# Performance work log

Measured on AMD Instinct MI355X. Metric: run time of the kernel, lower is better.

Reference implementation:

```python
import jax, jax.numpy as jnp
import numpy as np

B, S, D, NH, NKV, HD = 1, 2048, 4096, 32, 8, 128
SCALE = HD ** -0.5


def setup_inputs() -> dict:
    key = jax.random.key(0)
    ks = jax.random.split(key, 5)
    sd = D ** -0.5
    x = jax.random.normal(ks[0], (B, S, D), jnp.float32)
    Wq = jax.random.normal(ks[1], (D, NH * HD), jnp.float32) * sd
    Wk = jax.random.normal(ks[2], (D, NKV * HD), jnp.float32) * sd
    Wv = jax.random.normal(ks[3], (D, NKV * HD), jnp.float32) * sd
    Wo = jax.random.normal(ks[4], (NH * HD, D), jnp.float32) * sd
    # real rotary tables (rotate-half convention), shape [S, HD]
    inv_freq = 1.0 / (10000.0 ** (np.arange(0, HD, 2, dtype=np.float64) / HD))
    ang = np.outer(np.arange(S, dtype=np.float64), inv_freq)  # [S, HD//2]
    emb = np.concatenate([ang, ang], axis=-1)  # [S, HD]
    cos = jnp.asarray(np.cos(emb), jnp.float32)
    sin = jnp.asarray(np.sin(emb), jnp.float32)
    return dict(x=x, Wq=Wq, Wk=Wk, Wv=Wv, Wo=Wo, cos=cos, sin=sin)


def _rope(t, cos, sin):
    # t: [B,S,H,HD]; cos/sin: [S,HD]
    c = cos[None, :, None, :]
    s = sin[None, :, None, :]
    t1, t2 = jnp.split(t, 2, axis=-1)
    rot = jnp.concatenate([-t2, t1], axis=-1)
    return t * c + rot * s


def _to_i8(t):
    # per-vector absmax quantization over last dim
    scale = 127.0 / jnp.clip(jnp.max(jnp.abs(t), axis=-1, keepdims=True), 1e-5, None)
    q = jnp.clip(jnp.round(t * scale), -128.0, 127.0).astype(jnp.int8)
    return q, scale


def reference(x, Wq, Wk, Wv, Wo, cos, sin):
    q = (x @ Wq).reshape(B, S, NH, HD)
    k = (x @ Wk).reshape(B, S, NKV, HD)
    v = (x @ Wv).reshape(B, S, NKV, HD)
    q = _rope(q, cos, sin)
    k = _rope(k, cos, sin)
    q_i8, q_s = _to_i8(q)          # [B,S,NH,HD], [B,S,NH,1]
    k_i8, k_s = _to_i8(k)          # [B,S,NKV,HD], [B,S,NKV,1]
    rep = NH // NKV                # GQA expansion
    k_i8 = jnp.repeat(k_i8, rep, axis=2)
    k_s = jnp.repeat(k_s, rep, axis=2)
    v = jnp.repeat(v, rep, axis=2)
    # int8 QK^T accumulated in int32 (exact), then per-vector dequant
    scores = jnp.einsum('bshd,bthd->bhst', q_i8, k_i8,
                        preferred_element_type=jnp.int32).astype(jnp.float32)
    q_st = jnp.transpose(q_s, (0, 2, 1, 3))            # [B,NH,S,1]
    k_st = jnp.transpose(k_s, (0, 2, 3, 1))            # [B,NH,1,S]
    scores = scores * (SCALE / (q_st * k_st))
    # causal mask (seq > 1, no cache so total == S)
    mask = jnp.triu(jnp.full((S, S), -jnp.inf, jnp.float32), k=1)
    scores = scores + mask
    attn = jax.nn.softmax(scores, axis=-1)             # [B,NH,S,S]
    out = jnp.einsum('bhst,bthd->bshd', attn, v).reshape(B, S, NH * HD)
    return out @ Wo
```

## Files before the change

kernel.cpp:

```cpp
#include <hip/hip_runtime.h>
#include <hip/hip_bf16.h>

#define S_LEN 2048
#define DMODEL 4096
#define NH 32
#define NKV 8
#define HD 128
#define NQKV 6144
#define VOFF (DMODEL + NKV * HD)
#define ATT_SCALE_L2E 0.1275175213528852f

typedef __bf16 bf16x8 __attribute__((ext_vector_type(8)));
typedef __bf16 bf16x4 __attribute__((ext_vector_type(4)));
typedef float f32x4 __attribute__((ext_vector_type(4)));

template <bool B> struct BoolC { static constexpr bool value = B; };

__device__ __forceinline__ unsigned short f2b(float f) {
  union { float f; unsigned u; } a; a.f = f;
  unsigned u = a.u;
  return (unsigned short)((u + 0x7FFFu + ((u >> 16) & 1u)) >> 16);
}
__device__ __forceinline__ float b2f(unsigned short u) {
  union { unsigned u; float f; } a; a.u = (unsigned)u << 16; return a.f;
}

__device__ __forceinline__ void gl16(const unsigned short* g, unsigned short* l) {
  __builtin_amdgcn_global_load_lds(
      (const __attribute__((address_space(1))) unsigned int*)g,
      (__attribute__((address_space(3))) unsigned int*)l, 16, 0, 0);
}

__global__ __launch_bounds__(256) void k_prep(const float* __restrict__ x,
                                              const float* __restrict__ Wq,
                                              const float* __restrict__ Wk,
                                              const float* __restrict__ Wv,
                                              const float* __restrict__ Wo,
                                              unsigned short* __restrict__ xb,
                                              unsigned short* __restrict__ wqkv_t,
                                              unsigned short* __restrict__ wo_t) {
  __shared__ float tile[64][65];
  const int id = blockIdx.x;
  if (id >= 10240) {
    int i = (id - 10240) * 256 + threadIdx.x;
    float4 v = ((const float4*)x)[i];
    ushort4 o;
    o.x = f2b(v.x); o.y = f2b(v.y); o.z = f2b(v.z); o.w = f2b(v.w);
    ((ushort4*)xb)[i] = o;
    return;
  }
  const float* W;
  unsigned short* Wt;
  int N, bx, by;
  if (id < 4096)      { W = Wq; Wt = wqkv_t;                         N = 4096; bx = id & 63;          by = id >> 6; }
  else if (id < 5120) { W = Wk; Wt = wqkv_t + (size_t)4096 * 4096;   N = 1024; bx = (id - 4096) & 63; by = (id - 4096) >> 6; }
  else if (id < 6144) { W = Wv; Wt = wqkv_t + (size_t)5120 * 4096;   N = 1024; bx = (id - 5120) & 63; by = (id - 5120) >> 6; }
  else                { W = Wo; Wt = wo_t;                           N = 4096; bx = (id - 6144) & 63; by = (id - 6144) >> 6; }
  const int k0 = bx * 64, n0 = by * 64;
  const int tx = threadIdx.x & 31, ty = threadIdx.x >> 5;
#pragma unroll
  for (int i = 0; i < 8; ++i) {
    int k = ty + i * 8;
    const float* src = W + (size_t)(k0 + k) * N + n0;
    tile[k][tx] = src[tx];
    tile[k][tx + 32] = src[tx + 32];
  }
  __syncthreads();
  int kq = threadIdx.x & 15, nb = threadIdx.x >> 4;
#pragma unroll
  for (int i = 0; i < 4; ++i) {
    int n = nb + i * 16;
    ushort4 o;
    o.x = f2b(tile[kq * 4 + 0][n]);
    o.y = f2b(tile[kq * 4 + 1][n]);
    o.z = f2b(tile[kq * 4 + 2][n]);
    o.w = f2b(tile[kq * 4 + 3][n]);
    *(ushort4*)&Wt[(size_t)(n0 + n) * 4096 + k0 + kq * 4] = o;
  }
}

__global__ __launch_bounds__(256) void k_post(const unsigned short* __restrict__ qkv,
                                              const float* __restrict__ cost,
                                              const float* __restrict__ sint,
                                              unsigned short* __restrict__ q_int,
                                              float* __restrict__ q_ds_t,
                                              unsigned short* __restrict__ k_int,
                                              float* __restrict__ k_ds_t,
                                              unsigned short* __restrict__ v_t) {
  __shared__ unsigned short tile[64][65];
  const int id = blockIdx.x;
  if (id < 20480) {
    int y = id >> 11, s = id & 2047;
    int wv = threadIdx.x >> 6, l = threadIdx.x & 63;
    int hh = y * 4 + wv;
    const unsigned short* row = qkv + (size_t)s * NQKV;
    int off = (hh < NH) ? hh * HD : DMODEL + (hh - NH) * HD;
    float t1 = b2f(row[off + l]), t2 = b2f(row[off + 64 + l]);
    float c1 = cost[s * HD + l],      sn1 = sint[s * HD + l];
    float c2 = cost[s * HD + 64 + l], sn2 = sint[s * HD + 64 + l];
    float o1 = t1 * c1 - t2 * sn1;
    float o2 = t2 * c2 + t1 * sn2;
    float amax = fmaxf(fabsf(o1), fabsf(o2));
#pragma unroll
    for (int m = 1; m < 64; m <<= 1) amax = fmaxf(amax, __shfl_xor(amax, m));
    amax = fmaxf(amax, 1e-5f);
    float scale = 127.0f / amax;
    float dscale = amax * (1.0f / 127.0f);
    float v1 = fminf(fmaxf(rintf(o1 * scale), -128.f), 127.f);
    float v2 = fminf(fmaxf(rintf(o2 * scale), -128.f), 127.f);
    if (hh < NH) {
      unsigned short* dst = q_int + ((size_t)s * NH + hh) * HD;
      dst[l] = f2b(v1); dst[l + 64] = f2b(v2);
      if (l == 0) q_ds_t[(size_t)hh * S_LEN + s] = dscale;
    } else {
      int kh = hh - NH;
      unsigned short* dst = k_int + ((size_t)s * NKV + kh) * HD;
      dst[l] = f2b(v1); dst[l + 64] = f2b(v2);
      if (l == 0) k_ds_t[(size_t)kh * S_LEN + s] = dscale;
    }
    return;
  }
  int vid = id - 20480;
  int s0 = (vid & 31) * 64, d0 = ((vid >> 5) & 1) * 64, kvh = vid >> 6;
  int tx = threadIdx.x & 63, ty = threadIdx.x >> 6;
#pragma unroll
  for (int i = 0; i < 16; ++i) {
    int s = ty + i * 4;
    tile[s][tx] = qkv[(size_t)(s0 + s) * NQKV + VOFF + kvh * HD + d0 + tx];
  }
  __syncthreads();
#pragma unroll
  for (int i = 0; i < 16; ++i) {
    int d = ty + i * 4;
    v_t[((size_t)kvh * HD + d0 + d) * S_LEN + s0 + tx] = tile[tx][d];
  }
}

template <int FN, bool BF16OUT>
__global__ __launch_bounds__(512, 4) void k_g128(const unsigned short* __restrict__ A,
                                                 const unsigned short* __restrict__ B,
                                                 void* __restrict__ Cv,
                                                 int M, int N, int K) {
  extern __shared__ __align__(16) unsigned short smem[];
  char* Sc = (char*)smem;
  const int tid = threadIdx.x;
  const int wvid = tid >> 6, l = tid & 63;
  const int wm = wvid >> 2, wn = wvid & 3;
  const int l15 = l & 15, l4 = l >> 4;

  const int cpx = gridDim.x >> 3;
  const int swz = (blockIdx.x & 7) * cpx + (blockIdx.x >> 3);
  const int mtiles = M >> 7;
  const int m0 = (swz % mtiles) * 128;
  const int n0 = (swz / mtiles) * (FN * 64);

  const int NT = K >> 6;

  const int rsw = (l15 & 7) << 4;
  const int a_base = (wm * 64 + l15) * 128;
  const int b_base = (wn * FN * 16 + l15) * 128;
  const int c0 = (l4 * 16) ^ rsw;
  const int c1 = (64 + l4 * 16) ^ rsw;

  const int srow = l >> 3;
  const int st_k8 = (l & 7) ^ (srow & 7);

  auto stA = [&](int tt) {
    if (tt >= NT) return;
    const unsigned short* g = A + (size_t)(m0 + wvid * 8 + srow) * K + tt * 64 + st_k8 * 8;
    char* lb = Sc + (tt & 1) * 16384 + wvid * 1024;
#pragma unroll
    for (int j = 0; j < 2; ++j)
      gl16(g + (size_t)(j * 64) * K, (unsigned short*)(lb + j * 8192));
  };
  auto stB = [&](int tt) {
    if (tt >= NT) return;
    const unsigned short* g = B + (size_t)(n0 + wvid * 8 + srow) * K + tt * 64 + st_k8 * 8;
    char* lb = Sc + 32768 + (tt & 1) * (FN * 8192) + wvid * 1024;
#pragma unroll
    for (int j = 0; j < FN; ++j)
      gl16(g + (size_t)(j * 64) * K, (unsigned short*)(lb + j * 8192));
  };

  f32x4 acc[4][FN] = {};

  stA(0); stB(0); stA(1);
  if (NT > 1) asm volatile("s_waitcnt vmcnt(2)" ::: "memory");
  else        asm volatile("s_waitcnt vmcnt(0)" ::: "memory");
  __builtin_amdgcn_s_barrier();

  for (int t = 0; t < NT; ++t) {
    const char* Ab = Sc + (t & 1) * 16384;
    const char* Bb = Sc + 32768 + (t & 1) * (FN * 8192);
    stB(t + 1);
    bf16x8 a[4], b[FN];
#pragma unroll
    for (int fm = 0; fm < 4; ++fm) a[fm] = *(const bf16x8*)(Ab + a_base + fm * 2048 + c0);
#pragma unroll
    for (int fn = 0; fn < FN; ++fn) b[fn] = *(const bf16x8*)(Bb + b_base + fn * 2048 + c0);
    __builtin_amdgcn_s_setprio(1);
#pragma unroll
    for (int fm = 0; fm < 4; ++fm)
#pragma unroll
      for (int fn = 0; fn < FN; ++fn)
        acc[fm][fn] = __builtin_amdgcn_mfma_f32_16x16x32_bf16(a[fm], b[fn], acc[fm][fn], 0, 0, 0);
    __builtin_amdgcn_s_setprio(0);
#pragma unroll
    for (int fm = 0; fm < 4; ++fm) a[fm] = *(const bf16x8*)(Ab + a_base + fm * 2048 + c1);
#pragma unroll
    for (int fn = 0; fn < FN; ++fn) b[fn] = *(const bf16x8*)(Bb + b_base + fn * 2048 + c1);
    __builtin_amdgcn_s_setprio(1);
#pragma unroll
    for (int fm = 0; fm < 4; ++fm)
#pragma unroll
      for (int fn = 0; fn < FN; ++fn)
        acc[fm][fn] = __builtin_amdgcn_mfma_f32_16x16x32_bf16(a[fm], b[fn], acc[fm][fn], 0, 0, 0);
    __builtin_amdgcn_s_setprio(0);
    __builtin_amdgcn_s_barrier();
    stA(t + 2);
    if (t + 1 < NT) {
      if (t + 1 == NT - 1) asm volatile("s_waitcnt vmcnt(0)" ::: "memory");
      else                 asm volatile("s_waitcnt vmcnt(2)" ::: "memory");
      __builtin_amdgcn_s_barrier();
    }
  }

#pragma unroll
  for (int fm = 0; fm < 4; ++fm) {
    int row0 = m0 + wm * 64 + fm * 16 + l4 * 4;
#pragma unroll
    for (int fn = 0; fn < FN; ++fn) {
      int col = n0 + wn * FN * 16 + fn * 16 + l15;
#pragma unroll
      for (int r = 0; r < 4; ++r) {
        if constexpr (BF16OUT)
          ((unsigned short*)Cv)[(size_t)(row0 + r) * N + col] = f2b(acc[fm][fn][r]);
        else
          ((float*)Cv)[(size_t)(row0 + r) * N + col] = acc[fm][fn][r];
      }
    }
  }
}

__global__ __launch_bounds__(512, 4) void k_attn(const unsigned short* __restrict__ q_int,
                                                 const float* __restrict__ q_ds_t,
                                                 const unsigned short* __restrict__ k_int,
                                                 const float* __restrict__ k_ds_t,
                                                 const unsigned short* __restrict__ v_t,
                                                 unsigned short* __restrict__ o_bf) {
  __shared__ __align__(16) unsigned short K_lds[2][8192];
  __shared__ __align__(16) unsigned short V_lds[2][8192];
  __shared__ __align__(16) unsigned short P_lds[8][1024];

  const int bid = blockIdx.x;
  const int kvh = bid & 7;
  const int qt = 63 - (bid >> 3);
  const int tid = threadIdx.x, wv = tid >> 6, l = tid & 63;
  const int l15 = l & 15, l4 = l >> 4;
  const int h = kvh * 4 + (wv & 3);
  const int rh = wv >> 2;

  auto stage = [&](int b, int kt) {
    const unsigned short* kB = k_int + (size_t)kt * 64 * (NKV * HD) + kvh * HD;
    const unsigned short* vB = v_t + (size_t)kvh * HD * S_LEN + (size_t)kt * 64;
#pragma unroll
    for (int j = 0; j < 2; ++j) {
      int wi = j * 8 + wv;
      int slot = wi * 64 + l;
      int key = slot >> 4;
      int colb = ((slot & 15) * 16) ^ ((key & 7) << 4);
      gl16(kB + key * (NKV * HD) + (colb >> 1), &K_lds[b][wi * 512]);
      int d = slot >> 3;
      int ckb = ((slot & 7) * 16) ^ ((d & 7) << 4);
      gl16(vB + (size_t)d * S_LEN + (ckb >> 1), &V_lds[b][wi * 512]);
    }
  };

  const int qrow_lo = qt * 32 + rh * 16;
  const int qg = qrow_lo + l15;
  const int crow = qrow_lo + l4 * 4;

  bf16x8 qf[4];
  {
    const unsigned short* qp = q_int + ((size_t)qg * NH + h) * HD + l4 * 8;
#pragma unroll
    for (int kd = 0; kd < 4; ++kd) qf[kd] = *(const bf16x8*)(qp + kd * 32);
  }
  const float qsS = ATT_SCALE_L2E * q_ds_t[(size_t)h * S_LEN + qg];

  float m_run = -3.0e38f, l_run = 0.f;
  f32x4 o_acc[8] = {};

  const int nkt = (qt >> 1) + 1;
  stage(0, 0);
  __syncthreads();

  const int psw = (l15 & 7) << 4;

  auto tileBody = [&](auto mc, int kt) {
    constexpr bool MASKED = decltype(mc)::value;
    const int cur = kt & 1;
    f32x4 ksd[4];
    {
      const f32x4* kdp = (const f32x4*)(k_ds_t + (size_t)kvh * S_LEN + kt * 64 + l4 * 4);
#pragma unroll
      for (int nt = 0; nt < 4; ++nt) ksd[nt] = kdp[nt * 4];
    }
    if (kt + 1 < nkt) stage(cur ^ 1, kt + 1);

    f32x4 sacc[4] = {};
#pragma unroll
    for (int nt = 0; nt < 4; ++nt) {
      int key = nt * 16 + l15;
#pragma unroll
      for (int kd = 0; kd < 4; ++kd) {
        int byte = key * 256 + kd * 64 + l4 * 16;
        byte ^= (key & 7) << 4;
        bf16x8 kf = *(const bf16x8*)((const char*)&K_lds[cur][0] + byte);
        sacc[nt] = __builtin_amdgcn_mfma_f32_16x16x32_bf16(kf, qf[kd], sacc[nt], 0, 0, 0);
      }
    }

    float p[4][4];
    float tmax = -3.0e38f;
#pragma unroll
    for (int nt = 0; nt < 4; ++nt) {
#pragma unroll
      for (int r = 0; r < 4; ++r) {
        float sc = sacc[nt][r] * (qsS * ksd[nt][r]);
        if constexpr (MASKED) {
          int keyg = kt * 64 + nt * 16 + l4 * 4 + r;
          sc = (keyg <= qg) ? sc : -3.0e38f;
        }
        p[nt][r] = sc;
        tmax = fmaxf(tmax, sc);
      }
    }
    tmax = fmaxf(tmax, __shfl_xor(tmax, 16));
    tmax = fmaxf(tmax, __shfl_xor(tmax, 32));

    float nm = fmaxf(m_run, tmax);
    bool need = tmax > m_run + 11.0f;
    if (__ballot(need)) {
      float corr = __builtin_amdgcn_exp2f(m_run - nm);
      m_run = nm;
      l_run *= corr;
      float cq[4];
#pragma unroll
      for (int r = 0; r < 4; ++r) cq[r] = __shfl(corr, (l & 48) | (l4 * 4 + r));
#pragma unroll
      for (int dt = 0; dt < 8; ++dt)
#pragma unroll
        for (int r = 0; r < 4; ++r) o_acc[dt][r] *= cq[r];
    }

    float psum = 0.f;
#pragma unroll
    for (int nt = 0; nt < 4; ++nt)
#pragma unroll
      for (int r = 0; r < 4; ++r) {
        float e = __builtin_amdgcn_exp2f(p[nt][r] - m_run);
        p[nt][r] = e;
        psum += e;
      }
    psum += __shfl_xor(psum, 16);
    psum += __shfl_xor(psum, 32);
    l_run += psum;

#pragma unroll
    for (int nt = 0; nt < 4; ++nt) {
      bf16x4 pk;
      pk[0] = (__bf16)p[nt][0]; pk[1] = (__bf16)p[nt][1];
      pk[2] = (__bf16)p[nt][2]; pk[3] = (__bf16)p[nt][3];
      int bw = l15 * 128 + ((nt * 32 + l4 * 8) ^ psw);
      *(bf16x4*)((char*)&P_lds[wv][0] + bw) = pk;
    }
    bf16x8 pa[2];
#pragma unroll
    for (int kc = 0; kc < 2; ++kc) {
      int br = l15 * 128 + ((kc * 64 + l4 * 16) ^ psw);
      pa[kc] = *(const bf16x8*)((const char*)&P_lds[wv][0] + br);
    }

#pragma unroll
    for (int dt = 0; dt < 8; ++dt) {
      int d = dt * 16 + l15;
      int swzv = (d & 7) << 4;
#pragma unroll
      for (int kc = 0; kc < 2; ++kc) {
        int byte = d * 128 + ((kc * 64 + l4 * 16) ^ swzv);
        bf16x8 vb = *(const bf16x8*)((const char*)&V_lds[cur][0] + byte);
        o_acc[dt] = __builtin_amdgcn_mfma_f32_16x16x32_bf16(pa[kc], vb, o_acc[dt], 0, 0, 0);
      }
    }
    __syncthreads();
  };

  for (int kt = 0; kt + 1 < nkt; ++kt) tileBody(BoolC<false>{}, kt);
  tileBody(BoolC<true>{}, nkt - 1);

  float inv = 1.0f / l_run;
  float invq[4];
#pragma unroll
  for (int r = 0; r < 4; ++r) invq[r] = __shfl(inv, (l & 48) | (l4 * 4 + r));
#pragma unroll
  for (int dt = 0; dt < 8; ++dt)
#pragma unroll
    for (int r = 0; r < 4; ++r)
      o_bf[(size_t)(crow + r) * (NH * HD) + h * HD + dt * 16 + l15] =
          f2b(o_acc[dt][r] * invq[r]);
}

extern "C" void kernel_launch(void* const* d_in, const int* in_sizes, int n_in,
                              void* d_out, int out_size, void* d_ws, size_t ws_size,
                              hipStream_t stream) {
  const float* x    = (const float*)d_in[0];
  const float* Wq   = (const float*)d_in[1];
  const float* Wk   = (const float*)d_in[2];
  const float* Wv   = (const float*)d_in[3];
  const float* Wo   = (const float*)d_in[4];
  const float* cost = (const float*)d_in[5];
  const float* sint = (const float*)d_in[6];
  float* out = (float*)d_out;
  char* ws = (char*)d_ws;

  unsigned short* xb     = (unsigned short*)(ws);
  unsigned short* wqkv_t = (unsigned short*)(ws + 16777216);
  unsigned short* wo_t   = (unsigned short*)(ws + 67108864);
  unsigned short* qkv    = (unsigned short*)(ws + 100663296);
  unsigned short* q_int  = (unsigned short*)(ws + 150994944);
  unsigned short* k_int  = (unsigned short*)(ws + 167772160);
  float*          q_ds_t = (float*)(ws + 176160768);
  float*          k_ds_t = (float*)(ws + 176422912);
  unsigned short* o_bf   = (unsigned short*)(ws + 176488448);
  unsigned short* v_t    = (unsigned short*)(ws);

  hipFuncSetAttribute((const void*)k_g128<3, true>,
                      hipFuncAttributeMaxDynamicSharedMemorySize, 81920);
  hipFuncSetAttribute((const void*)k_g128<2, false>,
                      hipFuncAttributeMaxDynamicSharedMemorySize, 65536);

  k_prep<<<dim3(18432), 256, 0, stream>>>(x, Wq, Wk, Wv, Wo, xb, wqkv_t, wo_t);
  k_g128<3, true><<<dim3(512), 512, 81920, stream>>>(xb, wqkv_t, qkv, 2048, 6144, 4096);
  k_post<<<dim3(20992), 256, 0, stream>>>(qkv, cost, sint, q_int, q_ds_t, k_int, k_ds_t, v_t);
  k_attn<<<dim3(512), 512, 0, stream>>>(q_int, q_ds_t, k_int, k_ds_t, v_t, o_bf);
  k_g128<2, false><<<dim3(512), 512, 65536, stream>>>(o_bf, wo_t, out, 2048, 4096, 4096);
}
```

Baseline: 314.2 us.

## Use intra-block K-split waves for the output projection GEMM

```diff
diff --git a/kernel.cpp b/kernel.cpp
--- a/kernel.cpp
+++ b/kernel.cpp
@@ -136,11 +136,11 @@
   }
 }
 
-template <int FN, bool BF16OUT>
-__global__ __launch_bounds__(512, 4) void k_g128(const unsigned short* __restrict__ A,
-                                                 const unsigned short* __restrict__ B,
-                                                 void* __restrict__ Cv,
-                                                 int M, int N, int K) {
+__global__ __launch_bounds__(512, 4) void k_g128x3(const unsigned short* __restrict__ A,
+                                                   const unsigned short* __restrict__ B,
+                                                   unsigned short* __restrict__ C,
+                                                   int M, int N, int K) {
+  constexpr int FN = 3;
   extern __shared__ __align__(16) unsigned short smem[];
   char* Sc = (char*)smem;
   const int tid = threadIdx.x;
@@ -232,11 +232,108 @@
     for (int fn = 0; fn < FN; ++fn) {
       int col = n0 + wn * FN * 16 + fn * 16 + l15;
 #pragma unroll
-      for (int r = 0; r < 4; ++r) {
-        if constexpr (BF16OUT)
-          ((unsigned short*)Cv)[(size_t)(row0 + r) * N + col] = f2b(acc[fm][fn][r]);
-        else
-          ((float*)Cv)[(size_t)(row0 + r) * N + col] = acc[fm][fn][r];
+      for (int r = 0; r < 4; ++r)
+        C[(size_t)(row0 + r) * N + col] = f2b(acc[fm][fn][r]);
+    }
+  }
+}
+
+__global__ __launch_bounds__(512, 4) void k_gksplit(const unsigned short* __restrict__ A,
+                                                    const unsigned short* __restrict__ B,
+                                                    float* __restrict__ C,
+                                                    int M, int N, int K) {
+  extern __shared__ __align__(16) unsigned short smem[];
+  char* Sc = (char*)smem;
+  const int tid = threadIdx.x;
+  const int wvid = tid >> 6, l = tid & 63;
+  const int wm = wvid & 1, wn = (wvid >> 1) & 1, wk = wvid >> 2;
+  const int l15 = l & 15, l4 = l >> 4;
+
+  const int cpx = gridDim.x >> 3;
+  const int swz = (blockIdx.x & 7) * cpx + (blockIdx.x >> 3);
+  const int mtiles = M >> 7;
+  const int m0 = (swz % mtiles) * 128;
+  const int n0 = (swz / mtiles) * 128;
+
+  const int NT = K >> 6;
+
+  const int rsw = (l15 & 7) << 4;
+  const int a_base = (wm * 64 + l15) * 128;
+  const int b_base = (wn * 64 + l15) * 128;
+  const int ck = (wk * 64 + l4 * 16) ^ rsw;
+
+  const int srow = l >> 3;
+  const int st_k8 = (l & 7) ^ (srow & 7);
+
+  auto stA = [&](int tt) {
+    if (tt >= NT) return;
+    const unsigned short* g = A + (size_t)(m0 + wvid * 8 + srow) * K + tt * 64 + st_k8 * 8;
+    char* lb = Sc + (tt & 1) * 16384 + wvid * 1024;
+#pragma unroll
+    for (int j = 0; j < 2; ++j)
+      gl16(g + (size_t)(j * 64) * K, (unsigned short*)(lb + j * 8192));
+  };
+  auto stB = [&](int tt) {
+    if (tt >= NT) return;
+    const unsigned short* g = B + (size_t)(n0 + wvid * 8 + srow) * K + tt * 64 + st_k8 * 8;
+    char* lb = Sc + 32768 + (tt & 1) * 16384 + wvid * 1024;
+#pragma unroll
+    for (int j = 0; j < 2; ++j)
+      gl16(g + (size_t)(j * 64) * K, (unsigned short*)(lb + j * 8192));
+  };
+
+  f32x4 acc[4][4] = {};
+
+  stA(0); stB(0); stA(1);
+  if (NT > 1) asm volatile("s_waitcnt vmcnt(2)" ::: "memory");
+  else        asm volatile("s_waitcnt vmcnt(0)" ::: "memory");
+  __builtin_amdgcn_s_barrier();
+
+  for (int t = 0; t < NT; ++t) {
+    const char* Ab = Sc + (t & 1) * 16384;
+    const char* Bb = Sc + 32768 + (t & 1) * 16384;
+    stB(t + 1);
+    bf16x8 a[4], b[4];
+#pragma unroll
+    for (int fm = 0; fm < 4; ++fm) a[fm] = *(const bf16x8*)(Ab + a_base + fm * 2048 + ck);
+#pragma unroll
+    for (int fn = 0; fn < 4; ++fn) b[fn] = *(const bf16x8*)(Bb + b_base + fn * 2048 + ck);
+    __builtin_amdgcn_s_setprio(1);
+#pragma unroll
+    for (int fm = 0; fm < 4; ++fm)
+#pragma unroll
+      for (int fn = 0; fn < 4; ++fn)
+        acc[fm][fn] = __builtin_amdgcn_mfma_f32_16x16x32_bf16(a[fm], b[fn], acc[fm][fn], 0, 0, 0);
+    __builtin_amdgcn_s_setprio(0);
+    __builtin_amdgcn_s_barrier();
+    stA(t + 2);
+    if (t + 1 < NT) {
+      if (t + 1 == NT - 1) asm volatile("s_waitcnt vmcnt(0)" ::: "memory");
+      else                 asm volatile("s_waitcnt vmcnt(2)" ::: "memory");
+      __builtin_amdgcn_s_barrier();
+    }
+  }
+
+  char* xch = Sc + (wm * 2 + wn) * 16384;
+  if (wk == 1) {
+#pragma unroll
+    for (int fm = 0; fm < 4; ++fm)
+#pragma unroll
+      for (int fn = 0; fn < 4; ++fn)
+        *(f32x4*)(xch + (fm * 4 + fn) * 1024 + l * 16) = acc[fm][fn];
+  }
+  __syncthreads();
+  if (wk == 0) {
+#pragma unroll
+    for (int fm = 0; fm < 4; ++fm) {
+      int row0 = m0 + wm * 64 + fm * 16 + l4 * 4;
+#pragma unroll
+      for (int fn = 0; fn < 4; ++fn) {
+        f32x4 o = *(const f32x4*)(xch + (fm * 4 + fn) * 1024 + l * 16);
+        int col = n0 + wn * 64 + fn * 16 + l15;
+#pragma unroll
+        for (int r = 0; r < 4; ++r)
+          C[(size_t)(row0 + r) * N + col] = acc[fm][fn][r] + o[r];
       }
     }
   }
@@ -435,14 +532,14 @@
   unsigned short* o_bf   = (unsigned short*)(ws + 176488448);
   unsigned short* v_t    = (unsigned short*)(ws);
 
-  hipFuncSetAttribute((const void*)k_g128<3, true>,
+  hipFuncSetAttribute((const void*)k_g128x3,
                       hipFuncAttributeMaxDynamicSharedMemorySize, 81920);
-  hipFuncSetAttribute((const void*)k_g128<2, false>,
+  hipFuncSetAttribute((const void*)k_gksplit,
                       hipFuncAttributeMaxDynamicSharedMemorySize, 65536);
 
   k_prep<<<dim3(18432), 256, 0, stream>>>(x, Wq, Wk, Wv, Wo, xb, wqkv_t, wo_t);
-  k_g128<3, true><<<dim3(512), 512, 81920, stream>>>(xb, wqkv_t, qkv, 2048, 6144, 4096);
+  k_g128x3<<<dim3(512), 512, 81920, stream>>>(xb, wqkv_t, qkv, 2048, 6144, 4096);
   k_post<<<dim3(20992), 256, 0, stream>>>(qkv, cost, sint, q_int, q_ds_t, k_int, k_ds_t, v_t);
   k_attn<<<dim3(512), 512, 0, stream>>>(q_int, q_ds_t, k_int, k_ds_t, v_t, o_bf);
-  k_g128<2, false><<<dim3(512), 512, 65536, stream>>>(o_bf, wo_t, out, 2048, 4096, 4096);
-}
+  k_gksplit<<<dim3(512), 512, 65536, stream>>>(o_bf, wo_t, out, 2048, 4096, 4096);
+}
```

After: 306.6 us (median of 2 runs). -2.4%, faster.
